# Kernel optimization log

Measured on AMD Instinct MI355X. Metric: run time of the kernel, lower is better.

## Reference

```python
import jax, jax.numpy as jnp
import numpy as np

N, E = 50000, 800000
H_IN, H, L = 256, 128, 3
EPS = 1e-5  # BatchNorm1d default eps


def setup_inputs() -> dict:
    key = jax.random.key(0)
    ks = jax.random.split(key, 8)
    x = jax.random.normal(ks[0], (N, H_IN), jnp.float32)
    edge_index = jax.random.randint(ks[1], (2, E), 0, N, dtype=jnp.int32)

    def glorot(k, fi, fo):
        lim = np.sqrt(6.0 / (fi + fo)).astype(np.float32)
        return jax.random.uniform(k, (fi, fo), jnp.float32, -lim, lim)

    W_feat = glorot(ks[2], H_IN, H)
    b_feat = jnp.zeros((H,), jnp.float32)
    wkeys = jax.random.split(ks[3], L)
    Ws = jnp.stack([glorot(wkeys[i], H, H) for i in range(L)])
    bs = jnp.zeros((L, H), jnp.float32)
    # BN init per reset_parameters: weight=1, bias=1e-4
    bn_feat_g = jnp.ones((H_IN,), jnp.float32)
    bn_feat_b = jnp.full((H_IN,), 1e-4, jnp.float32)
    bn_g = jnp.ones((L, H), jnp.float32)
    bn_b = jnp.full((L, H), 1e-4, jnp.float32)
    return dict(x=x, edge_index=edge_index, bn_feat_g=bn_feat_g, bn_feat_b=bn_feat_b,
                W_feat=W_feat, b_feat=b_feat, bn_g=bn_g, bn_b=bn_b, Ws=Ws, bs=bs)


def _bn(x, gamma, beta):
    # training-mode BatchNorm1d: batch statistics over nodes, biased variance
    mu = x.mean(0)
    var = x.var(0)
    return (x - mu) * jax.lax.rsqrt(var + EPS) * gamma + beta


def _gcn_norm(edge_index, n):
    # add self-loops (fill value 1) + symmetric deg^-1/2 normalization
    row, col = edge_index[0], edge_index[1]
    loop = jnp.arange(n, dtype=row.dtype)
    row = jnp.concatenate([row, loop])
    col = jnp.concatenate([col, loop])
    deg = jax.ops.segment_sum(jnp.ones_like(row, jnp.float32), row, num_segments=n)
    dinv = jnp.where(deg > 0, jax.lax.rsqrt(deg), 0.0)
    return row, col, dinv[row] * dinv[col]


def _gcn(x, W, b, row, col, norm, n):
    x = x @ W                                   # [n, out]
    msg = x[row] * norm[:, None]                # gather + scale, [E+n, out]
    out = jax.ops.segment_sum(msg, col, num_segments=n)  # scatter-add
    return out + b


def reference(x, edge_index, bn_feat_g, bn_feat_b, W_feat, b_feat, bn_g, bn_b, Ws, bs):
    n = x.shape[0]
    row, col, norm = _gcn_norm(edge_index, n)   # same for every layer
    x = _bn(x, bn_feat_g, bn_feat_b)
    x = _gcn(x, W_feat, b_feat, row, col, norm, n)
    for i in range(L):
        x = _bn(x, bn_g[i], bn_b[i])
        x = _gcn(x, Ws[i], bs[i], row, col, norm, n)
    return x
```

## Files before the change

kernel.cpp:

```cpp
#include <hip/hip_runtime.h>
#include <hip/hip_bf16.h>

#define H_IN 256
#define H    128
#define BN_EPS 1e-5f
#define NCOPY 32
#define NSLICE 256
#define HSL 64
#define SMAX 5120
#define STATS_FLOATS (NCOPY * 2 * H_IN)
#define SBLK 1024
#define GEMMB 512
#define CH_SH 13
#define NBIN 2048

using u16 = unsigned short;
using u32 = unsigned int;
typedef __attribute__((ext_vector_type(8))) unsigned short us8;
typedef __attribute__((ext_vector_type(8))) short bf16x8;
typedef __attribute__((ext_vector_type(4))) float f32x4;

__device__ __forceinline__ float b2f(u16 u) {
    return __uint_as_float(((u32)u) << 16);
}
__device__ __forceinline__ u16 f2b(float f) {
    u32 u = __float_as_uint(f);
    u += 0x7FFF + ((u >> 16) & 1);
    return (u16)(u >> 16);
}

__global__ __launch_bounds__(256) void build_k(const int* __restrict__ row,
                                               const int* __restrict__ col,
                                               u32* __restrict__ hist_part,
                                               u32* __restrict__ bcnt_part,
                                               const float* __restrict__ x,
                                               u16* __restrict__ xb,
                                               float* __restrict__ statsA,
                                               int E, int total4, int QW, int qN) {
    extern __shared__ u32 smem[];
    int tid = threadIdx.x;
    int bx = blockIdx.x;
    if (bx < NSLICE) {
        u32* bcnt = smem;
        bcnt[tid] = 0;
        __syncthreads();
        int len = (E + NSLICE - 1) / NSLICE;
        int e0 = bx * len;
        int e1 = min(e0 + len, E);
        int e = e0 + tid;
        for (; e + 3 * 256 < e1; e += 4 * 256) {
            u32 c0 = (u32)col[e];
            u32 c1 = (u32)col[e + 256];
            u32 c2 = (u32)col[e + 512];
            u32 c3 = (u32)col[e + 768];
            atomicAdd(&bcnt[c0 >> 8], 1u);
            atomicAdd(&bcnt[c1 >> 8], 1u);
            atomicAdd(&bcnt[c2 >> 8], 1u);
            atomicAdd(&bcnt[c3 >> 8], 1u);
        }
        for (; e < e1; e += 256)
            atomicAdd(&bcnt[((u32)col[e]) >> 8], 1u);
        __syncthreads();
        bcnt_part[bx * 256 + tid] = bcnt[tid];
    } else if (bx < NSLICE + 4 * HSL) {
        int hb = bx - NSLICE;
        int s = hb >> 2;
        int qq = hb & 3;
        u32* hist = smem;
        for (int i = tid; i < QW; i += 256) hist[i] = 0;
        __syncthreads();
        int len = (E + HSL - 1) / HSL;
        int e0 = s * len;
        int e1 = min(e0 + len, E);
        int lo = qq * qN;
        int e = e0 + tid;
        for (; e + 3 * 256 < e1; e += 4 * 256) {
            int r0 = row[e] - lo;
            int r1 = row[e + 256] - lo;
            int r2 = row[e + 512] - lo;
            int r3 = row[e + 768] - lo;
            if ((u32)r0 < (u32)qN) atomicAdd(&hist[r0 >> 1], 1u << ((r0 & 1) << 4));
            if ((u32)r1 < (u32)qN) atomicAdd(&hist[r1 >> 1], 1u << ((r1 & 1) << 4));
            if ((u32)r2 < (u32)qN) atomicAdd(&hist[r2 >> 1], 1u << ((r2 & 1) << 4));
            if ((u32)r3 < (u32)qN) atomicAdd(&hist[r3 >> 1], 1u << ((r3 & 1) << 4));
        }
        for (; e < e1; e += 256) {
            int r = row[e] - lo;
            if ((u32)r < (u32)qN) atomicAdd(&hist[r >> 1], 1u << ((r & 1) << 4));
        }
        __syncthreads();
        u32* dst = hist_part + (size_t)hb * QW;
        for (int i = tid; i < QW; i += 256) dst[i] = hist[i];
    } else {
        float* sh = (float*)smem;
        const int K = H_IN;
        const int csz = 2 * H_IN;
        sh[tid] = 0.f;
        sh[tid + 256] = 0.f;
        __syncthreads();
        int sb = bx - NSLICE - 4 * HSL;
        int gid = sb * 256 + tid;
        int stride = SBLK * 256;
        int c0 = (tid * 4) & (H_IN - 1);
        float s0=0.f,s1=0.f,s2=0.f,s3=0.f, q0=0.f,q1=0.f,q2=0.f,q3=0.f;
        const float4* A4 = (const float4*)x;
        ushort4* X4 = (ushort4*)xb;
        auto proc = [&](int idx, float4 v) {
            ushort4 xv;
            xv.x = f2b(v.x); xv.y = f2b(v.y); xv.z = f2b(v.z); xv.w = f2b(v.w);
            X4[idx] = xv;
            s0 += v.x; q0 += v.x * v.x;
            s1 += v.y; q1 += v.y * v.y;
            s2 += v.z; q2 += v.z * v.z;
            s3 += v.w; q3 += v.w * v.w;
        };
        int i = gid;
        for (; i + 3 * stride < total4; i += 4 * stride) {
            float4 v0 = A4[i];
            float4 v1 = A4[i + stride];
            float4 v2 = A4[i + 2 * stride];
            float4 v3 = A4[i + 3 * stride];
            proc(i, v0);
            proc(i + stride, v1);
            proc(i + 2 * stride, v2);
            proc(i + 3 * stride, v3);
        }
        for (; i < total4; i += stride) proc(i, A4[i]);
        atomicAdd(&sh[c0],     s0); atomicAdd(&sh[K + c0],     q0);
        atomicAdd(&sh[c0 + 1], s1); atomicAdd(&sh[K + c0 + 1], q1);
        atomicAdd(&sh[c0 + 2], s2); atomicAdd(&sh[K + c0 + 2], q2);
        atomicAdd(&sh[c0 + 3], s3); atomicAdd(&sh[K + c0 + 3], q3);
        __syncthreads();
        float* dst = statsA + (size_t)(sb & (NCOPY - 1)) * csz;
        for (int i2 = tid; i2 < csz; i2 += 256) atomicAdd(&dst[i2], sh[i2]);
    }
}

__global__ __launch_bounds__(256) void prep_k(const int* __restrict__ row,
                                              const int* __restrict__ col,
                                              const u32* __restrict__ bcnt_part,
                                              u32* __restrict__ bbase,
                                              u32* __restrict__ ebuf,
                                              const u32* __restrict__ hist_part,
                                              float* __restrict__ dinv,
                                              const float* __restrict__ W,
                                              const float* __restrict__ stats_mc,
                                              const float* __restrict__ g,
                                              const float* __restrict__ bcoef,
                                              const float* __restrict__ bias,
                                              u16* __restrict__ Wt,
                                              float* __restrict__ bp,
                                              int E, int N, int DB, int QW, int qN) {
    int tid = threadIdx.x;
    int bx = blockIdx.x;
    if (bx < NSLICE) {
        __shared__ u32 sc[256];
        __shared__ u32 cur[256];
        int s = bx;
        u32 tot = 0, pre = 0;
        int t = 0;
        for (; t + 3 < NSLICE; t += 4) {
            u32 v0 = bcnt_part[(t    ) * 256 + tid];
            u32 v1 = bcnt_part[(t + 1) * 256 + tid];
            u32 v2 = bcnt_part[(t + 2) * 256 + tid];
            u32 v3 = bcnt_part[(t + 3) * 256 + tid];
            tot += v0 + v1 + v2 + v3;
            pre += (t < s ? v0 : 0) + (t + 1 < s ? v1 : 0) +
                   (t + 2 < s ? v2 : 0) + (t + 3 < s ? v3 : 0);
        }
        for (; t < NSLICE; ++t) {
            u32 v = bcnt_part[t * 256 + tid];
            tot += v;
            if (t < s) pre += v;
        }
        sc[tid] = tot;
        __syncthreads();
        for (int o = 1; o < 256; o <<= 1) {
            u32 xv = (tid >= o) ? sc[tid - o] : 0;
            __syncthreads();
            sc[tid] += xv;
            __syncthreads();
        }
        u32 base = sc[tid] - tot;
        if (s == 0) {
            bbase[tid] = base;
            if (tid == 255) bbase[256] = sc[255];
        }
        cur[tid] = base + pre;
        __syncthreads();
        int len = (E + NSLICE - 1) / NSLICE;
        int e0 = s * len;
        int e1 = min(e0 + len, E);
        for (int e = e0 + tid; e < e1; e += 256) {
            u32 r = (u32)row[e];
            u32 c = (u32)col[e];
            u32 pos = atomicAdd(&cur[c >> 8], 1u);
            ebuf[pos] = r | ((c & 255u) << 16);
        }
    } else if (bx < NSLICE + DB) {
        int w = (bx - NSLICE) * 256 + tid;
        if (w < 4 * QW) {
            int qq = w / QW;
            int lw = w - qq * QW;
            u32 v = 0;
            for (int s = 0; s < HSL; ++s)
                v += hist_part[(size_t)(s * 4 + qq) * QW + lw];
            int n = qq * qN + 2 * lw;
            if (n < N)     dinv[n]     = rsqrtf((float)(v & 0xFFFF) + 1.0f);
            if (n + 1 < N) dinv[n + 1] = rsqrtf((float)(v >> 16) + 1.0f);
        }
    } else {
        int j = bx - NSLICE - DB;
        int k = tid;
        const int K = H_IN;
        const int csz = 2 * H_IN;
        float sum = 0.f, sumsq = 0.f;
#pragma unroll
        for (int c = 0; c < NCOPY; ++c) {
            sum   += stats_mc[(size_t)c * csz + k];
            sumsq += stats_mc[(size_t)c * csz + K + k];
        }
        float mu = sum / (float)N;
        float var = sumsq / (float)N - mu * mu;
        float sK = g[k] * rsqrtf(var + BN_EPS);
        float tK = bcoef[k] - mu * sK;
        float w = W[(size_t)k * H + j];
        Wt[(size_t)j * K + k] = f2b(sK * w);
        __shared__ float red[256];
        red[k] = tK * w;
        __syncthreads();
        for (int o = 128; o > 0; o >>= 1) {
            if (k < o) red[k] += red[k + o];
            __syncthreads();
        }
        if (k == 0) bp[j] = bias[j] + red[0];
    }
}

template<int KT, int WITH_SORT, int FOLD>
__global__ __launch_bounds__(256) void gemm_mfma_k(const u16* __restrict__ Ab,
                                                   const u16* __restrict__ Wt,
                                                   u16* __restrict__ Yb, int M,
                                                   float* __restrict__ stats_z,
                                                   const u32* __restrict__ ebuf,
                                                   const u32* __restrict__ bbase,
                                                   int* __restrict__ rowptr,
                                                   u16* __restrict__ esrc, int N,
                                                   const float* __restrict__ Wf,
                                                   const float* __restrict__ stats_mc,
                                                   const float* __restrict__ g,
                                                   const float* __restrict__ bb,
                                                   const float* __restrict__ bias,
                                                   float* __restrict__ bp) {
    int tid = threadIdx.x;
    __shared__ u16 wt[FOLD ? H : 1][136];
    if constexpr (WITH_SORT != 0) {
        if (blockIdx.x >= GEMMB) {
            __shared__ u32 est[SMAX];
            __shared__ u32 hist[NBIN], cur[NBIN];
            __shared__ u32 scanw[256];
            int b = blockIdx.x - GEMMB;
            u32 base = bbase[b];
            int size = (int)(bbase[b + 1] - base);
            int st = min(size, SMAX);
            for (int i = tid; i < NBIN; i += 256) hist[i] = 0;
            __syncthreads();
            for (int i = tid; i < st; i += 256) {
                u32 e = ebuf[base + i];
                est[i] = e;
                u32 bin = (((e >> 16) & 255u) << 3) | ((e & 0xFFFFu) >> CH_SH);
                atomicAdd(&hist[bin], 1u);
            }
            for (int i = SMAX + tid; i < size; i += 256) {
                u32 e = ebuf[base + i];
                u32 bin = (((e >> 16) & 255u) << 3) | ((e & 0xFFFFu) >> CH_SH);
                atomicAdd(&hist[bin], 1u);
            }
            __syncthreads();
            u32 loc[8];
            u32 run = 0;
#pragma unroll
            for (int i = 0; i < 8; ++i) { loc[i] = run; run += hist[tid * 8 + i]; }
            scanw[tid] = run;
            __syncthreads();
            for (int o = 1; o < 256; o <<= 1) {
                u32 t2 = (tid >= o) ? scanw[tid - o] : 0;
                __syncthreads();
                scanw[tid] += t2;
                __syncthreads();
            }
            u32 off = scanw[tid] - run;
            int idx = (b << 8) + tid;
            if (idx <= N) rowptr[idx] = (int)(base + off);
#pragma unroll
            for (int i = 0; i < 8; ++i) cur[tid * 8 + i] = off + loc[i];
            __syncthreads();
            for (int i = tid; i < st; i += 256) {
                u32 e = est[i];
                u32 bin = (((e >> 16) & 255u) << 3) | ((e & 0xFFFFu) >> CH_SH);
                u32 pos = atomicAdd(&cur[bin], 1u);
                esrc[base + pos] = (u16)(e & 0xFFFFu);
            }
            for (int i = SMAX + tid; i < size; i += 256) {
                u32 e = ebuf[base + i];
                u32 bin = (((e >> 16) & 255u) << 3) | ((e & 0xFFFFu) >> CH_SH);
                u32 pos = atomicAdd(&cur[bin], 1u);
                esrc[base + pos] = (u16)(e & 0xFFFFu);
            }
            return;
        }
    }
    const int K = KT * 32;
    if constexpr (FOLD != 0) {
        __shared__ float s_sh[H], t_sh[H];
        __shared__ float red2[256];
        if (tid < H) {
            float sum = 0.f, sumsq = 0.f;
#pragma unroll
            for (int c = 0; c < NCOPY; ++c) {
                sum   += stats_mc[(size_t)c * (2 * H) + tid];
                sumsq += stats_mc[(size_t)c * (2 * H) + H + tid];
            }
            float mu = sum / (float)N;
            float var = sumsq / (float)N - mu * mu;
            float sv = g[tid] * rsqrtf(var + BN_EPS);
            s_sh[tid] = sv;
            t_sh[tid] = bb[tid] - mu * sv;
        }
        __syncthreads();
        int j = tid & 127, half = tid >> 7;
        float bpacc = 0.f;
        for (int it = 0; it < 64; ++it) {
            int k = it * 2 + half;
            float w = Wf[(size_t)k * H + j];
            wt[j][k] = f2b(s_sh[k] * w);
            bpacc += t_sh[k] * w;
        }
        red2[tid] = bpacc;
        __syncthreads();
        if (blockIdx.x == 0 && tid < H) bp[tid] = bias[tid] + red2[tid] + red2[tid + 128];
    }
    if (stats_z && blockIdx.x == 0) {
        for (int i = tid; i < STATS_FLOATS; i += 256) stats_z[i] = 0.f;
    }
    int w = tid >> 6;
    int lane = tid & 63;
    int m16 = lane & 15;
    int q = lane >> 4;

    bf16x8 bfrag[KT][2];
#pragma unroll
    for (int t = 0; t < KT; ++t)
#pragma unroll
        for (int p = 0; p < 2; ++p) {
            int ncol = 32 * w + 16 * p + m16;
            if constexpr (FOLD != 0)
                bfrag[t][p] = *(const bf16x8*)(&wt[ncol][32 * t + 8 * q]);
            else
                bfrag[t][p] = *(const bf16x8*)(Wt + (size_t)ncol * K + 32 * t + 8 * q);
        }

    int nchunk = M >> 4;
    for (int c = blockIdx.x; c < nchunk; c += GEMMB) {
        int m0 = c << 4;
        const u16* Arow = Ab + (size_t)(m0 + m16) * K + 8 * q;
        bf16x8 afrag[KT];
#pragma unroll
        for (int t = 0; t < KT; ++t)
            afrag[t] = *(const bf16x8*)(Arow + 32 * t);
        f32x4 acc0 = {0.f, 0.f, 0.f, 0.f}, acc1 = {0.f, 0.f, 0.f, 0.f};
#pragma unroll
        for (int t = 0; t < KT; ++t) {
            acc0 = __builtin_amdgcn_mfma_f32_16x16x32_bf16(afrag[t], bfrag[t][0], acc0, 0, 0, 0);
            acc1 = __builtin_amdgcn_mfma_f32_16x16x32_bf16(afrag[t], bfrag[t][1], acc1, 0, 0, 0);
        }
        u16* Crow = Yb + (size_t)(m0 + q * 4) * H + 32 * w + m16;
#pragma unroll
        for (int i = 0; i < 4; ++i) {
            Crow[(size_t)i * H]      = f2b(acc0[i]);
            Crow[(size_t)i * H + 16] = f2b(acc1[i]);
        }
    }
}

__global__ __launch_bounds__(256) void csragg_k(const int* __restrict__ rowptr,
                                                const u16* __restrict__ esrc,
                                                const u16* __restrict__ Yb,
                                                const float* __restrict__ dinv,
                                                const float* __restrict__ bp,
                                                u16* __restrict__ Ob,
                                                float* __restrict__ Of,
                                                float* __restrict__ stats_mc,
                                                int do_stats, int N) {
    __shared__ float sh[1024];
    int tid = threadIdx.x;
    int node = blockIdx.x * 16 + (tid >> 4);
    int fl = tid & 15;
    float o[8] = {0.f,0.f,0.f,0.f,0.f,0.f,0.f,0.f};
    if (node < N) {
        const us8* Y8 = (const us8*)Yb;
        float dn = dinv[node];
        float acc[8];
        {
            us8 ys = Y8[(size_t)node * 16 + fl];
#pragma unroll
            for (int j = 0; j < 8; ++j) acc[j] = dn * b2f(ys[j]);
        }
        int s = rowptr[node], e = rowptr[node + 1];
        int p = s;
        for (; p + 3 < e; p += 4) {
            int s0 = esrc[p], s1 = esrc[p + 1], s2 = esrc[p + 2], s3 = esrc[p + 3];
            float n0 = dinv[s0], n1 = dinv[s1], n2 = dinv[s2], n3 = dinv[s3];
            us8 v0 = Y8[(size_t)s0 * 16 + fl];
            us8 v1 = Y8[(size_t)s1 * 16 + fl];
            us8 v2 = Y8[(size_t)s2 * 16 + fl];
            us8 v3 = Y8[(size_t)s3 * 16 + fl];
#pragma unroll
            for (int j = 0; j < 8; ++j) acc[j] += n0 * b2f(v0[j]);
#pragma unroll
            for (int j = 0; j < 8; ++j) acc[j] += n1 * b2f(v1[j]);
#pragma unroll
            for (int j = 0; j < 8; ++j) acc[j] += n2 * b2f(v2[j]);
#pragma unroll
            for (int j = 0; j < 8; ++j) acc[j] += n3 * b2f(v3[j]);
        }
        for (; p < e; ++p) {
            int s0 = esrc[p];
            float n0 = dinv[s0];
            us8 v0 = Y8[(size_t)s0 * 16 + fl];
#pragma unroll
            for (int j = 0; j < 8; ++j) acc[j] += n0 * b2f(v0[j]);
        }
        float4 b0 = ((const float4*)bp)[fl * 2];
        float4 b1 = ((const float4*)bp)[fl * 2 + 1];
        o[0] = b0.x + dn * acc[0]; o[1] = b0.y + dn * acc[1];
        o[2] = b0.z + dn * acc[2]; o[3] = b0.w + dn * acc[3];
        o[4] = b1.x + dn * acc[4]; o[5] = b1.y + dn * acc[5];
        o[6] = b1.z + dn * acc[6]; o[7] = b1.w + dn * acc[7];
        if (Of) {
            float4* O4 = (float4*)Of;
            O4[(size_t)node * 32 + fl * 2]     = make_float4(o[0], o[1], o[2], o[3]);
            O4[(size_t)node * 32 + fl * 2 + 1] = make_float4(o[4], o[5], o[6], o[7]);
        } else {
            us8 ov;
#pragma unroll
            for (int j = 0; j < 8; ++j) ov[j] = f2b(o[j]);
            *(us8*)(Ob + (size_t)node * H + fl * 8) = ov;
        }
    }
    if (do_stats) {
        float sv[16];
#pragma unroll
        for (int j = 0; j < 8; ++j) { sv[j] = o[j]; sv[8 + j] = o[j] * o[j]; }
#pragma unroll
        for (int j = 0; j < 16; ++j) {
            sv[j] += __shfl_xor(sv[j], 16, 64);
            sv[j] += __shfl_xor(sv[j], 32, 64);
        }
        int lane = tid & 63, wv = tid >> 6;
        if (lane < 16) {
            float* base = sh + wv * 256;
#pragma unroll
            for (int j = 0; j < 8; ++j) {
                base[fl * 8 + j]       = sv[j];
                base[128 + fl * 8 + j] = sv[8 + j];
            }
        }
        __syncthreads();
        float v = sh[tid] + sh[256 + tid] + sh[512 + tid] + sh[768 + tid];
        atomicAdd(&stats_mc[(size_t)(blockIdx.x & (NCOPY - 1)) * (2 * H) + tid], v);
    }
}

extern "C" void kernel_launch(void* const* d_in, const int* in_sizes, int n_in,
                              void* d_out, int out_size, void* d_ws, size_t ws_size,
                              hipStream_t stream) {
    const float* x     = (const float*)d_in[0];
    const int*   ei    = (const int*)d_in[1];
    const float* bnfg  = (const float*)d_in[2];
    const float* bnfb  = (const float*)d_in[3];
    const float* Wfeat = (const float*)d_in[4];
    const float* bfeat = (const float*)d_in[5];
    const float* bng   = (const float*)d_in[6];
    const float* bnb   = (const float*)d_in[7];
    const float* Ws    = (const float*)d_in[8];
    const float* bs    = (const float*)d_in[9];

    int N = in_sizes[0] / H_IN;
    int E = in_sizes[1] / 2;
    const int* row = ei;
    const int* col = ei + E;

    int NB = (N + 255) >> 8;
    int QW = (N + 7) / 8;
    int qN = 2 * QW;
    int DB = (4 * QW + 255) / 256;

    char* p = (char*)d_ws;
    auto alloc = [&](size_t bytes) { char* r = p; p += (bytes + 63) & ~size_t(63); return r; };
    float* statsA    = (float*)alloc(STATS_FLOATS * 4);
    float* statsB    = (float*)alloc(STATS_FLOATS * 4);
    float* dinv      = (float*)alloc((size_t)N * 4);
    u16*   Wt        = (u16*)alloc(H_IN * H * 2);
    float* bp        = (float*)alloc(H * 4);
    u32*   hist_part = (u32*)alloc((size_t)4 * HSL * QW * 4);
    u32*   bcnt_part = (u32*)alloc(NSLICE * 256 * 4);
    u32*   bbase     = (u32*)alloc(257 * 4);
    int*   rowptr    = (int*)alloc((size_t)(N + 1) * 4);
    u32*   ebuf      = (u32*)alloc((size_t)E * 4);
    u16*   esrc      = (u16*)alloc((size_t)E * 2);
    u16*   xb        = (u16*)alloc((size_t)N * H_IN * 2);
    u16*   Yb        = (u16*)alloc((size_t)N * H * 2);
    u16*   ACTb      = (u16*)alloc((size_t)N * H * 2);

    float* out = (float*)d_out;

    hipMemsetAsync(statsA, 0, (size_t)(2 * STATS_FLOATS) * 4, stream);

    size_t lds_bytes = (size_t)QW * 4;
    if (lds_bytes < 2 * H_IN * 4) lds_bytes = 2 * H_IN * 4;

    build_k<<<NSLICE + 4 * HSL + SBLK, 256, lds_bytes, stream>>>(row, col, hist_part,
                                                                 bcnt_part, x, xb, statsA,
                                                                 E, N * H_IN / 4, QW, qN);
    prep_k<<<NSLICE + DB + H, 256, 0, stream>>>(row, col, bcnt_part, bbase, ebuf,
                                                hist_part, dinv,
                                                Wfeat, statsA, bnfg, bnfb, bfeat, Wt, bp,
                                                E, N, DB, QW, qN);
    gemm_mfma_k<8, 1, 0><<<GEMMB + NB, 256, 0, stream>>>(xb, Wt, Yb, N, nullptr,
                                                         ebuf, bbase, rowptr, esrc, N,
                                                         nullptr, nullptr, nullptr,
                                                         nullptr, nullptr, nullptr);
    csragg_k<<<(N + 15) / 16, 256, 0, stream>>>(rowptr, esrc, Yb, dinv, bp,
                                                ACTb, nullptr, statsB, 1, N);

    for (int l = 1; l < 4; ++l) {
        const float* W    = Ws + (size_t)(l - 1) * H * H;
        const float* bias = bs + (size_t)(l - 1) * H;
        const float* g    = bng + (size_t)(l - 1) * H;
        const float* bb   = bnb + (size_t)(l - 1) * H;
        float* sfold   = (l & 1) ? statsB : statsA;
        float* szero   = (l == 1) ? statsA : (l == 2) ? statsB : nullptr;
        float* starget = ((l + 1) & 1) ? statsB : statsA;

        gemm_mfma_k<4, 0, 1><<<GEMMB, 256, 0, stream>>>(ACTb, nullptr, Yb, N, szero,
                                                        nullptr, nullptr, nullptr, nullptr, N,
                                                        W, sfold, g, bb, bias, bp);
        csragg_k<<<(N + 15) / 16, 256, 0, stream>>>(rowptr, esrc, Yb, dinv, bp,
                                                    ACTb, (l == 3) ? out : nullptr,
                                                    starget, (l < 3) ? 1 : 0, N);
    }
}
```

Measured before the change: 344.1 us.

## Fuse GEMM, sort and aggregation layers into one cooperative persistent kernel

Replaces the chain of per-layer GEMM and CSR aggregation launches with one cooperative persistent kernel. Inside it, phases are separated by atomic grid barriers and each phase uses grid-stride loops. The aim is to remove kernel launch gaps and tail effects between the eight dependent stages. In exchange, the grid is capped by occupancy (up to 4 blocks per CU), grid barriers add spin overhead, and the large static LDS may reduce aggregation occupancy. A fallback multi-kernel path is kept in case the cooperative launch is unavailable.

```diff
diff --git a/kernel.cpp b/kernel.cpp
--- a/kernel.cpp
+++ b/kernel.cpp
@@ -10,9 +10,10 @@
 #define SMAX 5120
 #define STATS_FLOATS (NCOPY * 2 * H_IN)
 #define SBLK 1024
-#define GEMMB 512
 #define CH_SH 13
 #define NBIN 2048
+#define GEMMB 512
+#define SMEM_WORDS 9472
 
 using u16 = unsigned short;
 using u32 = unsigned int;
@@ -27,6 +28,19 @@
     u32 u = __float_as_uint(f);
     u += 0x7FFF + ((u >> 16) & 1);
     return (u16)(u >> 16);
+}
+
+__device__ __forceinline__ void gridbar(u32* cnt, u32 nblk) {
+    __syncthreads();
+    if (threadIdx.x == 0) {
+        __hip_atomic_fetch_add(cnt, 1u, __ATOMIC_ACQ_REL, __HIP_MEMORY_SCOPE_AGENT);
+        int guard = 0;
+        while (__hip_atomic_load(cnt, __ATOMIC_ACQUIRE, __HIP_MEMORY_SCOPE_AGENT) < nblk) {
+            __builtin_amdgcn_s_sleep(8);
+            if (++guard > 200000) break;
+        }
+    }
+    __syncthreads();
 }
 
 __global__ __launch_bounds__(256) void build_k(const int* __restrict__ row,
@@ -237,131 +251,29 @@
     }
 }
 
-template<int KT, int WITH_SORT, int FOLD>
-__global__ __launch_bounds__(256) void gemm_mfma_k(const u16* __restrict__ Ab,
-                                                   const u16* __restrict__ Wt,
-                                                   u16* __restrict__ Yb, int M,
-                                                   float* __restrict__ stats_z,
-                                                   const u32* __restrict__ ebuf,
-                                                   const u32* __restrict__ bbase,
-                                                   int* __restrict__ rowptr,
-                                                   u16* __restrict__ esrc, int N,
-                                                   const float* __restrict__ Wf,
-                                                   const float* __restrict__ stats_mc,
-                                                   const float* __restrict__ g,
-                                                   const float* __restrict__ bb,
-                                                   const float* __restrict__ bias,
-                                                   float* __restrict__ bp) {
+
+template<int KT, bool LDSW>
+__device__ __forceinline__ void gemm_core(const u16* __restrict__ Ab,
+                                          const u16* __restrict__ WtG,
+                                          const u16* wtL,
+                                          u16* __restrict__ Yb, int M,
+                                          int bx0, int stride) {
+    const int K = KT * 32;
     int tid = threadIdx.x;
-    __shared__ u16 wt[FOLD ? H : 1][136];
-    if constexpr (WITH_SORT != 0) {
-        if (blockIdx.x >= GEMMB) {
-            __shared__ u32 est[SMAX];
-            __shared__ u32 hist[NBIN], cur[NBIN];
-            __shared__ u32 scanw[256];
-            int b = blockIdx.x - GEMMB;
-            u32 base = bbase[b];
-            int size = (int)(bbase[b + 1] - base);
-            int st = min(size, SMAX);
-            for (int i = tid; i < NBIN; i += 256) hist[i] = 0;
-            __syncthreads();
-            for (int i = tid; i < st; i += 256) {
-                u32 e = ebuf[base + i];
-                est[i] = e;
-                u32 bin = (((e >> 16) & 255u) << 3) | ((e & 0xFFFFu) >> CH_SH);
-                atomicAdd(&hist[bin], 1u);
-            }
-            for (int i = SMAX + tid; i < size; i += 256) {
-                u32 e = ebuf[base + i];
-                u32 bin = (((e >> 16) & 255u) << 3) | ((e & 0xFFFFu) >> CH_SH);
-                atomicAdd(&hist[bin], 1u);
-            }
-            __syncthreads();
-            u32 loc[8];
-            u32 run = 0;
-#pragma unroll
-            for (int i = 0; i < 8; ++i) { loc[i] = run; run += hist[tid * 8 + i]; }
-            scanw[tid] = run;
-            __syncthreads();
-            for (int o = 1; o < 256; o <<= 1) {
-                u32 t2 = (tid >= o) ? scanw[tid - o] : 0;
-                __syncthreads();
-                scanw[tid] += t2;
-                __syncthreads();
-            }
-            u32 off = scanw[tid] - run;
-            int idx = (b << 8) + tid;
-            if (idx <= N) rowptr[idx] = (int)(base + off);
-#pragma unroll
-            for (int i = 0; i < 8; ++i) cur[tid * 8 + i] = off + loc[i];
-            __syncthreads();
-            for (int i = tid; i < st; i += 256) {
-                u32 e = est[i];
-                u32 bin = (((e >> 16) & 255u) << 3) | ((e & 0xFFFFu) >> CH_SH);
-                u32 pos = atomicAdd(&cur[bin], 1u);
-                esrc[base + pos] = (u16)(e & 0xFFFFu);
-            }
-            for (int i = SMAX + tid; i < size; i += 256) {
-                u32 e = ebuf[base + i];
-                u32 bin = (((e >> 16) & 255u) << 3) | ((e & 0xFFFFu) >> CH_SH);
-                u32 pos = atomicAdd(&cur[bin], 1u);
-                esrc[base + pos] = (u16)(e & 0xFFFFu);
-            }
-            return;
-        }
-    }
-    const int K = KT * 32;
-    if constexpr (FOLD != 0) {
-        __shared__ float s_sh[H], t_sh[H];
-        __shared__ float red2[256];
-        if (tid < H) {
-            float sum = 0.f, sumsq = 0.f;
-#pragma unroll
-            for (int c = 0; c < NCOPY; ++c) {
-                sum   += stats_mc[(size_t)c * (2 * H) + tid];
-                sumsq += stats_mc[(size_t)c * (2 * H) + H + tid];
-            }
-            float mu = sum / (float)N;
-            float var = sumsq / (float)N - mu * mu;
-            float sv = g[tid] * rsqrtf(var + BN_EPS);
-            s_sh[tid] = sv;
-            t_sh[tid] = bb[tid] - mu * sv;
-        }
-        __syncthreads();
-        int j = tid & 127, half = tid >> 7;
-        float bpacc = 0.f;
-        for (int it = 0; it < 64; ++it) {
-            int k = it * 2 + half;
-            float w = Wf[(size_t)k * H + j];
-            wt[j][k] = f2b(s_sh[k] * w);
-            bpacc += t_sh[k] * w;
-        }
-        red2[tid] = bpacc;
-        __syncthreads();
-        if (blockIdx.x == 0 && tid < H) bp[tid] = bias[tid] + red2[tid] + red2[tid + 128];
-    }
-    if (stats_z && blockIdx.x == 0) {
-        for (int i = tid; i < STATS_FLOATS; i += 256) stats_z[i] = 0.f;
-    }
-    int w = tid >> 6;
-    int lane = tid & 63;
-    int m16 = lane & 15;
-    int q = lane >> 4;
-
+    int w = tid >> 6, lane = tid & 63, m16 = lane & 15, q = lane >> 4;
     bf16x8 bfrag[KT][2];
 #pragma unroll
     for (int t = 0; t < KT; ++t)
 #pragma unroll
         for (int p = 0; p < 2; ++p) {
             int ncol = 32 * w + 16 * p + m16;
-            if constexpr (FOLD != 0)
-                bfrag[t][p] = *(const bf16x8*)(&wt[ncol][32 * t + 8 * q]);
+            if constexpr (LDSW)
+                bfrag[t][p] = *(const bf16x8*)(wtL + ncol * 136 + 32 * t + 8 * q);
             else
-                bfrag[t][p] = *(const bf16x8*)(Wt + (size_t)ncol * K + 32 * t + 8 * q);
-        }
-
+                bfrag[t][p] = *(const bf16x8*)(WtG + (size_t)ncol * K + 32 * t + 8 * q);
+        }
     int nchunk = M >> 4;
-    for (int c = blockIdx.x; c < nchunk; c += GEMMB) {
+    for (int c = bx0; c < nchunk; c += stride) {
         int m0 = c << 4;
         const u16* Arow = Ab + (size_t)(m0 + m16) * K + 8 * q;
         bf16x8 afrag[KT];
@@ -383,93 +295,282 @@
     }
 }
 
-__global__ __launch_bounds__(256) void csragg_k(const int* __restrict__ rowptr,
-                                                const u16* __restrict__ esrc,
-                                                const u16* __restrict__ Yb,
-                                                const float* __restrict__ dinv,
-                                                const float* __restrict__ bp,
-                                                u16* __restrict__ Ob,
-                                                float* __restrict__ Of,
-                                                float* __restrict__ stats_mc,
-                                                int do_stats, int N) {
-    __shared__ float sh[1024];
+__device__ __forceinline__ void sort_core(u32* smem, const u32* __restrict__ ebuf,
+                                          const u32* __restrict__ bbase,
+                                          int* __restrict__ rowptr,
+                                          u16* __restrict__ esrc, int N, int b) {
+    u32* est   = smem;
+    u32* hist  = smem + SMAX;
+    u32* cur   = hist + NBIN;
+    u32* scanw = cur + NBIN;
     int tid = threadIdx.x;
-    int node = blockIdx.x * 16 + (tid >> 4);
+    u32 base = bbase[b];
+    int size = (int)(bbase[b + 1] - base);
+    int st = min(size, SMAX);
+    for (int i = tid; i < NBIN; i += 256) hist[i] = 0;
+    __syncthreads();
+    for (int i = tid; i < st; i += 256) {
+        u32 e = ebuf[base + i];
+        est[i] = e;
+        u32 bin = (((e >> 16) & 255u) << 3) | ((e & 0xFFFFu) >> CH_SH);
+        atomicAdd(&hist[bin], 1u);
+    }
+    for (int i = SMAX + tid; i < size; i += 256) {
+        u32 e = ebuf[base + i];
+        u32 bin = (((e >> 16) & 255u) << 3) | ((e & 0xFFFFu) >> CH_SH);
+        atomicAdd(&hist[bin], 1u);
+    }
+    __syncthreads();
+    u32 loc[8];
+    u32 run = 0;
+#pragma unroll
+    for (int i = 0; i < 8; ++i) { loc[i] = run; run += hist[tid * 8 + i]; }
+    scanw[tid] = run;
+    __syncthreads();
+    for (int o = 1; o < 256; o <<= 1) {
+        u32 t2 = (tid >= o) ? scanw[tid - o] : 0;
+        __syncthreads();
+        scanw[tid] += t2;
+        __syncthreads();
+    }
+    u32 off = scanw[tid] - run;
+    int idx = (b << 8) + tid;
+    if (idx <= N) rowptr[idx] = (int)(base + off);
+#pragma unroll
+    for (int i = 0; i < 8; ++i) cur[tid * 8 + i] = off + loc[i];
+    __syncthreads();
+    for (int i = tid; i < st; i += 256) {
+        u32 e = est[i];
+        u32 bin = (((e >> 16) & 255u) << 3) | ((e & 0xFFFFu) >> CH_SH);
+        u32 pos = atomicAdd(&cur[bin], 1u);
+        esrc[base + pos] = (u16)(e & 0xFFFFu);
+    }
+    for (int i = SMAX + tid; i < size; i += 256) {
+        u32 e = ebuf[base + i];
+        u32 bin = (((e >> 16) & 255u) << 3) | ((e & 0xFFFFu) >> CH_SH);
+        u32 pos = atomicAdd(&cur[bin], 1u);
+        esrc[base + pos] = (u16)(e & 0xFFFFu);
+    }
+}
+
+__device__ __forceinline__ void csragg_core(u32* smem, const int* __restrict__ rowptr,
+                                            const u16* __restrict__ esrc,
+                                            const u16* __restrict__ Yb,
+                                            const float* __restrict__ dinv,
+                                            const float* __restrict__ bp,
+                                            u16* __restrict__ Ob,
+                                            float* __restrict__ Of,
+                                            float* __restrict__ stats_mc,
+                                            int do_stats, int N,
+                                            float* zbuf, int stride) {
+    float* sh = (float*)smem;
+    int tid = threadIdx.x;
+    if (zbuf && blockIdx.x == 0) {
+        for (int i = tid; i < STATS_FLOATS; i += 256) zbuf[i] = 0.f;
+    }
     int fl = tid & 15;
-    float o[8] = {0.f,0.f,0.f,0.f,0.f,0.f,0.f,0.f};
-    if (node < N) {
-        const us8* Y8 = (const us8*)Yb;
-        float dn = dinv[node];
-        float acc[8];
-        {
-            us8 ys = Y8[(size_t)node * 16 + fl];
-#pragma unroll
-            for (int j = 0; j < 8; ++j) acc[j] = dn * b2f(ys[j]);
-        }
-        int s = rowptr[node], e = rowptr[node + 1];
-        int p = s;
-        for (; p + 3 < e; p += 4) {
-            int s0 = esrc[p], s1 = esrc[p + 1], s2 = esrc[p + 2], s3 = esrc[p + 3];
-            float n0 = dinv[s0], n1 = dinv[s1], n2 = dinv[s2], n3 = dinv[s3];
-            us8 v0 = Y8[(size_t)s0 * 16 + fl];
-            us8 v1 = Y8[(size_t)s1 * 16 + fl];
-            us8 v2 = Y8[(size_t)s2 * 16 + fl];
-            us8 v3 = Y8[(size_t)s3 * 16 + fl];
-#pragma unroll
-            for (int j = 0; j < 8; ++j) acc[j] += n0 * b2f(v0[j]);
-#pragma unroll
-            for (int j = 0; j < 8; ++j) acc[j] += n1 * b2f(v1[j]);
-#pragma unroll
-            for (int j = 0; j < 8; ++j) acc[j] += n2 * b2f(v2[j]);
-#pragma unroll
-            for (int j = 0; j < 8; ++j) acc[j] += n3 * b2f(v3[j]);
-        }
-        for (; p < e; ++p) {
-            int s0 = esrc[p];
-            float n0 = dinv[s0];
-            us8 v0 = Y8[(size_t)s0 * 16 + fl];
-#pragma unroll
-            for (int j = 0; j < 8; ++j) acc[j] += n0 * b2f(v0[j]);
-        }
-        float4 b0 = ((const float4*)bp)[fl * 2];
-        float4 b1 = ((const float4*)bp)[fl * 2 + 1];
-        o[0] = b0.x + dn * acc[0]; o[1] = b0.y + dn * acc[1];
-        o[2] = b0.z + dn * acc[2]; o[3] = b0.w + dn * acc[3];
-        o[4] = b1.x + dn * acc[4]; o[5] = b1.y + dn * acc[5];
-        o[6] = b1.z + dn * acc[6]; o[7] = b1.w + dn * acc[7];
-        if (Of) {
-            float4* O4 = (float4*)Of;
-            O4[(size_t)node * 32 + fl * 2]     = make_float4(o[0], o[1], o[2], o[3]);
-            O4[(size_t)node * 32 + fl * 2 + 1] = make_float4(o[4], o[5], o[6], o[7]);
-        } else {
-            us8 ov;
-#pragma unroll
-            for (int j = 0; j < 8; ++j) ov[j] = f2b(o[j]);
-            *(us8*)(Ob + (size_t)node * H + fl * 8) = ov;
-        }
-    }
-    if (do_stats) {
-        float sv[16];
-#pragma unroll
-        for (int j = 0; j < 8; ++j) { sv[j] = o[j]; sv[8 + j] = o[j] * o[j]; }
-#pragma unroll
-        for (int j = 0; j < 16; ++j) {
-            sv[j] += __shfl_xor(sv[j], 16, 64);
-            sv[j] += __shfl_xor(sv[j], 32, 64);
-        }
-        int lane = tid & 63, wv = tid >> 6;
-        if (lane < 16) {
-            float* base = sh + wv * 256;
-#pragma unroll
-            for (int j = 0; j < 8; ++j) {
-                base[fl * 8 + j]       = sv[j];
-                base[128 + fl * 8 + j] = sv[8 + j];
-            }
-        }
-        __syncthreads();
-        float v = sh[tid] + sh[256 + tid] + sh[512 + tid] + sh[768 + tid];
-        atomicAdd(&stats_mc[(size_t)(blockIdx.x & (NCOPY - 1)) * (2 * H) + tid], v);
-    }
+    int NGRP = (N + 15) >> 4;
+    float4 b0 = ((const float4*)bp)[fl * 2];
+    float4 b1 = ((const float4*)bp)[fl * 2 + 1];
+    for (int grp = blockIdx.x; grp < NGRP; grp += stride) {
+        int node = grp * 16 + (tid >> 4);
+        float o[8] = {0.f,0.f,0.f,0.f,0.f,0.f,0.f,0.f};
+        if (node < N) {
+            const us8* Y8 = (const us8*)Yb;
+            float dn = dinv[node];
+            float acc[8];
+            {
+                us8 ys = Y8[(size_t)node * 16 + fl];
+#pragma unroll
+                for (int j = 0; j < 8; ++j) acc[j] = dn * b2f(ys[j]);
+            }
+            int s = rowptr[node], e = rowptr[node + 1];
+            int p = s;
+            for (; p + 3 < e; p += 4) {
+                int s0 = esrc[p], s1 = esrc[p + 1], s2 = esrc[p + 2], s3 = esrc[p + 3];
+                float n0 = dinv[s0], n1 = dinv[s1], n2 = dinv[s2], n3 = dinv[s3];
+                us8 v0 = Y8[(size_t)s0 * 16 + fl];
+                us8 v1 = Y8[(size_t)s1 * 16 + fl];
+                us8 v2 = Y8[(size_t)s2 * 16 + fl];
+                us8 v3 = Y8[(size_t)s3 * 16 + fl];
+#pragma unroll
+                for (int j = 0; j < 8; ++j) acc[j] += n0 * b2f(v0[j]);
+#pragma unroll
+                for (int j = 0; j < 8; ++j) acc[j] += n1 * b2f(v1[j]);
+#pragma unroll
+                for (int j = 0; j < 8; ++j) acc[j] += n2 * b2f(v2[j]);
+#pragma unroll
+                for (int j = 0; j < 8; ++j) acc[j] += n3 * b2f(v3[j]);
+            }
+            for (; p < e; ++p) {
+                int s0 = esrc[p];
+                float n0 = dinv[s0];
+                us8 v0 = Y8[(size_t)s0 * 16 + fl];
+#pragma unroll
+                for (int j = 0; j < 8; ++j) acc[j] += n0 * b2f(v0[j]);
+            }
+            o[0] = b0.x + dn * acc[0]; o[1] = b0.y + dn * acc[1];
+            o[2] = b0.z + dn * acc[2]; o[3] = b0.w + dn * acc[3];
+            o[4] = b1.x + dn * acc[4]; o[5] = b1.y + dn * acc[5];
+            o[6] = b1.z + dn * acc[6]; o[7] = b1.w + dn * acc[7];
+            if (Of) {
+                float4* O4 = (float4*)Of;
+                O4[(size_t)node * 32 + fl * 2]     = make_float4(o[0], o[1], o[2], o[3]);
+                O4[(size_t)node * 32 + fl * 2 + 1] = make_float4(o[4], o[5], o[6], o[7]);
+            } else {
+                us8 ov;
+#pragma unroll
+                for (int j = 0; j < 8; ++j) ov[j] = f2b(o[j]);
+                *(us8*)(Ob + (size_t)node * H + fl * 8) = ov;
+            }
+        }
+        if (do_stats) {
+            float sv[16];
+#pragma unroll
+            for (int j = 0; j < 8; ++j) { sv[j] = o[j]; sv[8 + j] = o[j] * o[j]; }
+#pragma unroll
+            for (int j = 0; j < 16; ++j) {
+                sv[j] += __shfl_xor(sv[j], 16, 64);
+                sv[j] += __shfl_xor(sv[j], 32, 64);
+            }
+            int lane = tid & 63, wv = tid >> 6;
+            if (lane < 16) {
+                float* base = sh + wv * 256;
+#pragma unroll
+                for (int j = 0; j < 8; ++j) {
+                    base[fl * 8 + j]       = sv[j];
+                    base[128 + fl * 8 + j] = sv[8 + j];
+                }
+            }
+            __syncthreads();
+            float v = sh[tid] + sh[256 + tid] + sh[512 + tid] + sh[768 + tid];
+            atomicAdd(&stats_mc[(size_t)(grp & (NCOPY - 1)) * (2 * H) + tid], v);
+            __syncthreads();
+        }
+    }
+}
+
+__device__ __forceinline__ void fold_gemm_core(u32* smem, const u16* __restrict__ ACTb,
+                                               u16* __restrict__ Yb,
+                                               const float* __restrict__ Wf,
+                                               const float* __restrict__ stats,
+                                               const float* __restrict__ g,
+                                               const float* __restrict__ bb,
+                                               const float* __restrict__ bias,
+                                               float* __restrict__ bp,
+                                               int N, int M, int stride) {
+    u16* wt = (u16*)smem;
+    float* s_sh = (float*)(smem + 8704);
+    float* t_sh = s_sh + 128;
+    float* red2 = t_sh + 128;
+    int tid = threadIdx.x;
+    if (tid < H) {
+        float sum = 0.f, sumsq = 0.f;
+#pragma unroll
+        for (int c = 0; c < NCOPY; ++c) {
+            sum   += stats[(size_t)c * (2 * H) + tid];
+            sumsq += stats[(size_t)c * (2 * H) + H + tid];
+        }
+        float mu = sum / (float)N;
+        float var = sumsq / (float)N - mu * mu;
+        float sv = g[tid] * rsqrtf(var + BN_EPS);
+        s_sh[tid] = sv;
+        t_sh[tid] = bb[tid] - mu * sv;
+    }
+    __syncthreads();
+    int j = tid & 127, half = tid >> 7;
+    float bpacc = 0.f;
+    for (int it = 0; it < 64; ++it) {
+        int k = it * 2 + half;
+        float w = Wf[(size_t)k * H + j];
+        wt[j * 136 + k] = f2b(s_sh[k] * w);
+        bpacc += t_sh[k] * w;
+    }
+    red2[tid] = bpacc;
+    __syncthreads();
+    if (blockIdx.x == 0 && tid < H) bp[tid] = bias[tid] + red2[tid] + red2[tid + 128];
+    gemm_core<4, true>(ACTb, nullptr, wt, Yb, M, blockIdx.x, stride);
+}
+
+struct MegaArgs {
+    const u16* xb; const u16* Wt; const float* bp0;
+    u16* Yb; u16* ACTb;
+    const u32* ebuf; const u32* bbase; int* rowptr; u16* esrc;
+    const float* dinv;
+    float* statsA; float* statsB; float* bp;
+    const float* Ws; const float* bs; const float* bng; const float* bnb;
+    float* out; u32* bar; int N; int NB;
+};
+
+__global__ __launch_bounds__(256, 2) void mega_k(MegaArgs a) {
+    __shared__ u32 smem[SMEM_WORDS];
+    int tid = threadIdx.x, bx = blockIdx.x;
+    int GRID = (int)gridDim.x;
+    int GB = GRID - a.NB;
+    if (bx < GB) {
+        if (bx == 0) {
+            for (int i = tid; i < STATS_FLOATS; i += 256) a.statsA[i] = 0.f;
+        }
+        gemm_core<8, false>(a.xb, a.Wt, nullptr, a.Yb, a.N, bx, GB);
+    } else {
+        sort_core(smem, a.ebuf, a.bbase, a.rowptr, a.esrc, a.N, bx - GB);
+    }
+    gridbar(a.bar + 0, GRID);
+    csragg_core(smem, a.rowptr, a.esrc, a.Yb, a.dinv, a.bp0, a.ACTb, nullptr,
+                a.statsB, 1, a.N, nullptr, GRID);
+    gridbar(a.bar + 1, GRID);
+    for (int l = 1; l < 4; ++l) {
+        const float* sin_ = (l & 1) ? a.statsB : a.statsA;
+        float* sout = (l & 1) ? a.statsA : a.statsB;
+        fold_gemm_core(smem, a.ACTb, a.Yb, a.Ws + (size_t)(l - 1) * H * H, sin_,
+                       a.bng + (l - 1) * H, a.bnb + (l - 1) * H, a.bs + (l - 1) * H,
+                       a.bp, a.N, a.N, GRID);
+        gridbar(a.bar + 2 * l, GRID);
+        csragg_core(smem, a.rowptr, a.esrc, a.Yb, a.dinv, a.bp,
+                    (l < 3) ? a.ACTb : nullptr, (l == 3) ? a.out : nullptr,
+                    sout, (l < 3) ? 1 : 0, a.N,
+                    (l == 1) ? a.statsB : nullptr, GRID);
+        if (l < 3) gridbar(a.bar + 2 * l + 1, GRID);
+    }
+}
+
+__global__ __launch_bounds__(256) void fb_gemm0sort_k(MegaArgs a) {
+    __shared__ u32 smem[SMEM_WORDS];
+    int bx = blockIdx.x, tid = threadIdx.x;
+    if (bx < GEMMB) {
+        if (bx == 0) {
+            for (int i = tid; i < STATS_FLOATS; i += 256) a.statsA[i] = 0.f;
+        }
+        gemm_core<8, false>(a.xb, a.Wt, nullptr, a.Yb, a.N, bx, GEMMB);
+    } else {
+        sort_core(smem, a.ebuf, a.bbase, a.rowptr, a.esrc, a.N, bx - GEMMB);
+    }
+}
+
+__global__ __launch_bounds__(256) void fb_foldgemm_k(const u16* __restrict__ ACTb,
+                                                     u16* __restrict__ Yb,
+                                                     const float* __restrict__ Wf,
+                                                     const float* __restrict__ stats,
+                                                     const float* __restrict__ g,
+                                                     const float* __restrict__ bb,
+                                                     const float* __restrict__ bias,
+                                                     float* __restrict__ bp, int N) {
+    __shared__ u32 smem[SMEM_WORDS];
+    fold_gemm_core(smem, ACTb, Yb, Wf, stats, g, bb, bias, bp, N, N, (int)gridDim.x);
+}
+
+__global__ __launch_bounds__(256) void fb_csragg_k(const int* __restrict__ rowptr,
+                                                   const u16* __restrict__ esrc,
+                                                   const u16* __restrict__ Yb,
+                                                   const float* __restrict__ dinv,
+                                                   const float* __restrict__ bp,
+                                                   u16* __restrict__ Ob,
+                                                   float* __restrict__ Of,
+                                                   float* __restrict__ stats_mc,
+                                                   int do_stats, int N, float* zbuf) {
+    __shared__ u32 smem[1024];
+    csragg_core(smem, rowptr, esrc, Yb, dinv, bp, Ob, Of, stats_mc,
+                do_stats, N, zbuf, (int)gridDim.x);
 }
 
 extern "C" void kernel_launch(void* const* d_in, const int* in_sizes, int n_in,
@@ -500,8 +601,10 @@
     auto alloc = [&](size_t bytes) { char* r = p; p += (bytes + 63) & ~size_t(63); return r; };
     float* statsA    = (float*)alloc(STATS_FLOATS * 4);
     float* statsB    = (float*)alloc(STATS_FLOATS * 4);
+    u32*   bar       = (u32*)alloc(64);
     float* dinv      = (float*)alloc((size_t)N * 4);
     u16*   Wt        = (u16*)alloc(H_IN * H * 2);
+    float* bp0       = (float*)alloc(H * 4);
     float* bp        = (float*)alloc(H * 4);
     u32*   hist_part = (u32*)alloc((size_t)4 * HSL * QW * 4);
     u32*   bcnt_part = (u32*)alloc(NSLICE * 256 * 4);
@@ -515,7 +618,7 @@
 
     float* out = (float*)d_out;
 
-    hipMemsetAsync(statsA, 0, (size_t)(2 * STATS_FLOATS) * 4, stream);
+    hipMemsetAsync(statsA, 0, (size_t)(2 * STATS_FLOATS) * 4 + 64, stream);
 
     size_t lds_bytes = (size_t)QW * 4;
     if (lds_bytes < 2 * H_IN * 4) lds_bytes = 2 * H_IN * 4;
@@ -525,29 +628,62 @@
                                                                  E, N * H_IN / 4, QW, qN);
     prep_k<<<NSLICE + DB + H, 256, 0, stream>>>(row, col, bcnt_part, bbase, ebuf,
                                                 hist_part, dinv,
-                                                Wfeat, statsA, bnfg, bnfb, bfeat, Wt, bp,
+                                                Wfeat, statsA, bnfg, bnfb, bfeat, Wt, bp0,
                                                 E, N, DB, QW, qN);
-    gemm_mfma_k<8, 1, 0><<<GEMMB + NB, 256, 0, stream>>>(xb, Wt, Yb, N, nullptr,
-                                                         ebuf, bbase, rowptr, esrc, N,
-                                                         nullptr, nullptr, nullptr,
-                                                         nullptr, nullptr, nullptr);
-    csragg_k<<<(N + 15) / 16, 256, 0, stream>>>(rowptr, esrc, Yb, dinv, bp,
-                                                ACTb, nullptr, statsB, 1, N);
-
-    for (int l = 1; l < 4; ++l) {
-        const float* W    = Ws + (size_t)(l - 1) * H * H;
-        const float* bias = bs + (size_t)(l - 1) * H;
-        const float* g    = bng + (size_t)(l - 1) * H;
-        const float* bb   = bnb + (size_t)(l - 1) * H;
-        float* sfold   = (l & 1) ? statsB : statsA;
-        float* szero   = (l == 1) ? statsA : (l == 2) ? statsB : nullptr;
-        float* starget = ((l + 1) & 1) ? statsB : statsA;
-
-        gemm_mfma_k<4, 0, 1><<<GEMMB, 256, 0, stream>>>(ACTb, nullptr, Yb, N, szero,
-                                                        nullptr, nullptr, nullptr, nullptr, N,
-                                                        W, sfold, g, bb, bias, bp);
-        csragg_k<<<(N + 15) / 16, 256, 0, stream>>>(rowptr, esrc, Yb, dinv, bp,
-                                                    ACTb, (l == 3) ? out : nullptr,
-                                                    starget, (l < 3) ? 1 : 0, N);
-    }
-}
+
+    MegaArgs ma;
+    ma.xb = xb; ma.Wt = Wt; ma.bp0 = bp0;
+    ma.Yb = Yb; ma.ACTb = ACTb;
+    ma.ebuf = ebuf; ma.bbase = bbase; ma.rowptr = rowptr; ma.esrc = esrc;
+    ma.dinv = dinv;
+    ma.statsA = statsA; ma.statsB = statsB; ma.bp = bp;
+    ma.Ws = Ws; ma.bs = bs; ma.bng = bng; ma.bnb = bnb;
+    ma.out = out; ma.bar = bar; ma.N = N; ma.NB = NB;
+
+    static int coop_state = -1;
+    static int coop_grid = 0;
+    bool used_coop = false;
+    if (coop_state != 0) {
+        if (coop_state == -1) {
+            int bpc = 0;
+            hipError_t qe = hipOccupancyMaxActiveBlocksPerMultiprocessor(&bpc, mega_k, 256, 0);
+            if (qe == hipSuccess && bpc >= 2) {
+                if (bpc > 4) bpc = 4;
+                coop_grid = bpc * 256;
+            } else {
+                coop_state = 0;
+            }
+        }
+        if (coop_state != 0 && coop_grid > NB + 64) {
+            void* kargs[] = { (void*)&ma };
+            hipError_t le = hipLaunchCooperativeKernel(mega_k, dim3(coop_grid), dim3(256),
+                                                       kargs, 0, stream);
+            if (le == hipSuccess) {
+                used_coop = true;
+                coop_state = 1;
+            } else {
+                coop_state = 0;
+                (void)hipGetLastError();
+            }
+        } else if (coop_state != 0) {
+            coop_state = 0;
+        }
+    }
+    if (!used_coop) {
+        fb_gemm0sort_k<<<GEMMB + NB, 256, 0, stream>>>(ma);
+        fb_csragg_k<<<(N + 15) / 16, 256, 0, stream>>>(rowptr, esrc, Yb, dinv, bp0,
+                                                       ACTb, nullptr, statsB, 1, N, nullptr);
+        for (int l = 1; l < 4; ++l) {
+            const float* sin_ = (l & 1) ? statsB : statsA;
+            float* sout = (l & 1) ? statsA : statsB;
+            fb_foldgemm_k<<<GEMMB, 256, 0, stream>>>(ACTb, Yb, Ws + (size_t)(l - 1) * H * H,
+                                                     sin_, bng + (l - 1) * H, bnb + (l - 1) * H,
+                                                     bs + (l - 1) * H, bp, N);
+            fb_csragg_k<<<(N + 15) / 16, 256, 0, stream>>>(rowptr, esrc, Yb, dinv, bp,
+                                                           (l < 3) ? ACTb : nullptr,
+                                                           (l == 3) ? out : nullptr,
+                                                           sout, (l < 3) ? 1 : 0, N,
+                                                           (l == 1) ? statsB : nullptr);
+        }
+    }
+}
```

Measured after the change: 925.3 us. 2.69x slower.
